# Optimization experiments

Hardware: AMD Instinct MI355X
Metric: run time of the kernel (lower is better)

## Reference

```python
import jax, jax.numpy as jnp
import numpy as np

# Static config (matches init_kwargs / spatial layout)
SHAPES = ((64, 64), (32, 32), (16, 16))   # (H, W) per level, bev=256 at /4,/8,/16
B, HEADS, LEVELS, POINTS, C = 2, 8, 3, 4, 256
HD = C // HEADS
NV = sum(h * w for h, w in SHAPES)        # 5376
NQ = NV
TP = HEADS * LEVELS * POINTS              # 96


def setup_inputs() -> dict:
    key = jax.random.key(0)
    ks = jax.random.split(key, 10)
    s = 1.0 / np.sqrt(C)
    inp = {
        'query': jax.random.normal(ks[0], (B, NQ, C), dtype=jnp.float32),
        'reference_points': jax.random.uniform(ks[1], (B, NQ, 2), dtype=jnp.float32),
        'value': jax.random.normal(ks[2], (B, NV, C), dtype=jnp.float32),
        'Wv': jax.random.normal(ks[3], (C, C), dtype=jnp.float32) * s,
        'bv': jnp.zeros((C,), dtype=jnp.float32),
        # offset proj: small scale so sampling stays local-ish (orig init is 0)
        'Woff': jax.random.normal(ks[4], (TP * 2, C), dtype=jnp.float32) * (0.02 * s),
        'boff': jnp.zeros((TP * 2,), dtype=jnp.float32),
        'Wa': jax.random.normal(ks[5], (TP, C), dtype=jnp.float32) * s,
        'ba': jnp.zeros((TP,), dtype=jnp.float32),
        'Wo': jax.random.normal(ks[6], (C, C), dtype=jnp.float32) * s,
        'bo': jnp.zeros((C,), dtype=jnp.float32),
    }
    return inp


def _msda(query, reference_points, value, Wv, bv, Woff, boff, Wa, ba, Wo, bo):
    Bb, nq, _ = query.shape
    # value projection -> per-head values
    v = (value @ Wv.T + bv).reshape(Bb, NV, HEADS, HD)
    # sampling offsets: (B, NQ, HEADS, LEVELS, POINTS, 2)
    off = (query @ Woff.T + boff).reshape(Bb, nq, HEADS, LEVELS, POINTS, 2)
    # attention weights: softmax over LEVELS*POINTS jointly
    a = (query @ Wa.T + ba).reshape(Bb, nq, HEADS, LEVELS * POINTS)
    a = jax.nn.softmax(a, axis=-1).reshape(Bb, nq, HEADS, LEVELS, POINTS)
    # sampling locations in [0,1] (clamp matches torch .clamp(0,1))
    loc = jnp.clip(reference_points[:, :, None, None, None, :] + off, 0.0, 1.0)

    out = jnp.zeros((Bb, HEADS, nq, HD), dtype=query.dtype)
    start = 0
    for lvl, (H, W) in enumerate(SHAPES):
        n = H * W
        # (B, HEADS, H*W, HD) flattened level feature map per head
        vl = jnp.transpose(v[:, start:start + n].reshape(Bb, H, W, HEADS, HD),
                           (0, 3, 1, 2, 4)).reshape(Bb, HEADS, n, HD)
        loc_l = loc[:, :, :, lvl]                     # (B, NQ, HEADS, K, 2)
        # align_corners=False unnormalization: ((g+1)*size - 1)/2 with g=2*loc-1
        x = loc_l[..., 0] * W - 0.5
        y = loc_l[..., 1] * H - 0.5
        x0 = jnp.floor(x)
        y0 = jnp.floor(y)
        wx1 = x - x0
        wy1 = y - y0
        x0i = x0.astype(jnp.int32)
        y0i = y0.astype(jnp.int32)
        acc = jnp.zeros((Bb, HEADS, nq * POINTS, HD), dtype=query.dtype)
        for dy in (0, 1):
            for dx in (0, 1):
                ix = x0i + dx
                iy = y0i + dy
                wgt = (wx1 if dx else 1.0 - wx1) * (wy1 if dy else 1.0 - wy1)
                # zero padding outside the map (padding_mode='zeros')
                valid = (ix >= 0) & (ix < W) & (iy >= 0) & (iy < H)
                idx = jnp.clip(iy, 0, H - 1) * W + jnp.clip(ix, 0, W - 1)
                idx_t = jnp.transpose(idx, (0, 2, 1, 3)).reshape(Bb, HEADS, nq * POINTS)
                g = jnp.take_along_axis(vl, idx_t[..., None], axis=2)  # (B,H,NQ*K,HD)
                w_t = jnp.transpose(wgt * valid.astype(wgt.dtype),
                                    (0, 2, 1, 3)).reshape(Bb, HEADS, nq * POINTS, 1)
                acc = acc + g * w_t
        aw = jnp.transpose(a[:, :, :, lvl], (0, 2, 1, 3)).reshape(Bb, HEADS, nq * POINTS, 1)
        out = out + (acc * aw).reshape(Bb, HEADS, nq, POINTS, HD).sum(axis=3)
        start += n
    out = jnp.transpose(out, (0, 2, 1, 3)).reshape(Bb, nq, C)
    return out @ Wo.T + bo


def reference(query, reference_points, value, Wv, bv, Woff, boff, Wa, ba, Wo, bo):
    return _msda(query, reference_points, value, Wv, bv, Woff, boff, Wa, ba, Wo, bo)
```

## Files before the change

### kernel.cpp

```cpp
#include <hip/hip_runtime.h>
#include <hip/hip_bf16.h>
#include <cmath>

#define BATCH   2
#define NQ      5376
#define NV      5376
#define CDIM    256
#define HEADS   8
#define HD      32
#define LEVELS  3
#define POINTS  4
#define TP      96
#define MROWS   (BATCH*NQ)
#define NOFF    (TP*2)
#define NQA     (NOFF+TP)

typedef __attribute__((ext_vector_type(8))) short bf16x8;
typedef __attribute__((ext_vector_type(4))) float f32x4;
typedef unsigned short u16;
typedef unsigned int   u32;

#define AS1 __attribute__((address_space(1)))
#define AS3 __attribute__((address_space(3)))

__device__ __forceinline__ void g2lds16(const void* g, void* l) {
    __builtin_amdgcn_global_load_lds((const AS1 void*)g, (AS3 void*)l, 16, 0, 0);
}

__device__ __forceinline__ u16 bf_of(float f) {
    union { __hip_bfloat16 h; u16 s; } u;
    u.h = __float2bfloat16(f);
    return u.s;
}
__device__ __forceinline__ float bf_back(u16 s) {
    return __uint_as_float((u32)s << 16);
}

__global__ __launch_bounds__(256) void split_vq_kernel(
    const float* __restrict__ value, const float* __restrict__ query,
    u16* __restrict__ vhi, u16* __restrict__ vlo,
    u16* __restrict__ qhi, int n4)
{
    int i = blockIdx.x * 256 + threadIdx.x;
    const float* src; u16* dh; u16* dl;
    if (i < n4) { src = value; dh = vhi; dl = vlo; }
    else        { src = query; dh = qhi; dl = nullptr; i -= n4; }
    const float4 v = reinterpret_cast<const float4*>(src)[i];
    ushort4 h;
    h.x = bf_of(v.x); h.y = bf_of(v.y); h.z = bf_of(v.z); h.w = bf_of(v.w);
    reinterpret_cast<ushort4*>(dh)[i] = h;
    if (dl) {
        ushort4 l;
        l.x = bf_of(v.x - bf_back(h.x));
        l.y = bf_of(v.y - bf_back(h.y));
        l.z = bf_of(v.z - bf_back(h.z));
        l.w = bf_of(v.w - bf_back(h.w));
        reinterpret_cast<ushort4*>(dl)[i] = l;
    }
}

__global__ __launch_bounds__(256) void split_w_kernel(
    const float* __restrict__ Wv, const float* __restrict__ Woff,
    const float* __restrict__ Wa, const float* __restrict__ Wo,
    u16* __restrict__ wv_hi, u16* __restrict__ wv_lo,
    u16* __restrict__ wqa_hi,
    u16* __restrict__ wo_hi, u16* __restrict__ wo_lo)
{
    const int i = blockIdx.x * 256 + threadIdx.x;
    const float* src; u16* dh; u16* dl; int j;
    if (i < 16384) {
        j = i; src = Wv + (size_t)j * 4; dh = wv_hi; dl = wv_lo;
    } else if (i < 34816) {
        j = i - 16384;
        const int row = j >> 6, c4 = j & 63;
        src = (row < NOFF) ? (Woff + (size_t)row * CDIM + c4 * 4)
                           : (Wa + (size_t)(row - NOFF) * CDIM + c4 * 4);
        dh = wqa_hi; dl = nullptr;
    } else {
        j = i - 34816; src = Wo + (size_t)j * 4; dh = wo_hi; dl = wo_lo;
    }
    const float4 v = *reinterpret_cast<const float4*>(src);
    ushort4 h;
    h.x = bf_of(v.x); h.y = bf_of(v.y); h.z = bf_of(v.z); h.w = bf_of(v.w);
    reinterpret_cast<ushort4*>(dh)[j] = h;
    if (dl) {
        ushort4 l;
        l.x = bf_of(v.x - bf_back(h.x));
        l.y = bf_of(v.y - bf_back(h.y));
        l.z = bf_of(v.z - bf_back(h.z));
        l.w = bf_of(v.w - bf_back(h.w));
        reinterpret_cast<ushort4*>(dl)[j] = l;
    }
}

#define GBM 64
#define GBN 64
#define GBK 32

template <int NPROD, int MODE>
__global__ __launch_bounds__(256) void gemm_split_kernel(
    const u16* __restrict__ Ah, const u16* __restrict__ Al,
    const u16* __restrict__ Bh, const u16* __restrict__ Bl,
    const float* __restrict__ bias, const float* __restrict__ bias2,
    void* __restrict__ Cout, void* __restrict__ Cout2,
    int M, int N, int K)
{
    __shared__ u16 sAh[GBM * GBK];
    __shared__ u16 sAl[GBM * GBK];
    __shared__ u16 sBh[GBN * GBK];
    __shared__ u16 sBl[GBN * GBK];

    const int m0 = blockIdx.x * GBM;
    const int n0 = blockIdx.y * GBN;
    const int tid  = threadIdx.x;
    const int lane = tid & 63;
    const int wave = tid >> 6;
    const int wr   = wave & 1;
    const int wc   = wave >> 1;
    const int qm   = lane & 15;
    const int quad = lane >> 4;

    f32x4 acc[2][2];
    #pragma unroll
    for (int i = 0; i < 2; ++i)
        #pragma unroll
        for (int j = 0; j < 2; ++j)
            acc[i][j] = (f32x4){0.f, 0.f, 0.f, 0.f};

    const int srow = (wave << 4) + (lane >> 2);
    const int sk   = (lane & 3) * 8;
    const int brc  = min(n0 + srow, N - 1);

    for (int k0 = 0; k0 < K; k0 += GBK) {
        const size_t ga = (size_t)(m0 + srow) * K + k0 + sk;
        const size_t gb = (size_t)brc * K + k0 + sk;
        g2lds16(Ah + ga, sAh + wave * 512);
        if (NPROD >= 2) g2lds16(Al + ga, sAl + wave * 512);
        g2lds16(Bh + gb, sBh + wave * 512);
        if (NPROD >= 3) g2lds16(Bl + gb, sBl + wave * 512);
        __syncthreads();

        bf16x8 fah[2], fal[2], fbh[2], fbl[2];
        #pragma unroll
        for (int x = 0; x < 2; ++x) {
            const int rm = wr * 32 + x * 16 + qm;
            const int rn = wc * 32 + x * 16 + qm;
            fah[x] = *reinterpret_cast<const bf16x8*>(&sAh[rm * GBK + quad * 8]);
            fbh[x] = *reinterpret_cast<const bf16x8*>(&sBh[rn * GBK + quad * 8]);
            if (NPROD >= 2)
                fal[x] = *reinterpret_cast<const bf16x8*>(&sAl[rm * GBK + quad * 8]);
            if (NPROD >= 3)
                fbl[x] = *reinterpret_cast<const bf16x8*>(&sBl[rn * GBK + quad * 8]);
        }
        #pragma unroll
        for (int mi = 0; mi < 2; ++mi)
            #pragma unroll
            for (int ni = 0; ni < 2; ++ni) {
                acc[mi][ni] = __builtin_amdgcn_mfma_f32_16x16x32_bf16(
                    fah[mi], fbh[ni], acc[mi][ni], 0, 0, 0);
                if (NPROD >= 2)
                    acc[mi][ni] = __builtin_amdgcn_mfma_f32_16x16x32_bf16(
                        fal[mi], fbh[ni], acc[mi][ni], 0, 0, 0);
                if (NPROD >= 3)
                    acc[mi][ni] = __builtin_amdgcn_mfma_f32_16x16x32_bf16(
                        fah[mi], fbl[ni], acc[mi][ni], 0, 0, 0);
            }
        __syncthreads();
    }

    #pragma unroll
    for (int mi = 0; mi < 2; ++mi) {
        #pragma unroll
        for (int ni = 0; ni < 2; ++ni) {
            const int n = n0 + wc * 32 + ni * 16 + qm;
            if (n >= N) continue;
            float bn;
            if (MODE == 2) bn = (n < NOFF) ? bias[n] : bias2[n - NOFF];
            else           bn = bias[n];
            #pragma unroll
            for (int r = 0; r < 4; ++r) {
                const int m = m0 + wr * 32 + mi * 16 + quad * 4 + r;
                const float val = acc[mi][ni][r] + bn;
                if (MODE == 0) {
                    reinterpret_cast<float*>(Cout)[(size_t)m * N + n] = val;
                } else if (MODE == 1) {
                    const int b = m / NV, rr = m - b * NV;
                    const int h = n >> 5, c = n & 31;
                    reinterpret_cast<u16*>(Cout)[
                        (((size_t)b * HEADS + h) * NV + rr) * HD + c] = bf_of(val);
                } else {
                    if (n < NOFF)
                        reinterpret_cast<float*>(Cout)[(size_t)m * NOFF + n] = val;
                    else
                        reinterpret_cast<float*>(Cout2)[(size_t)m * TP + (n - NOFF)] = val;
                }
            }
        }
    }
}

__global__ __launch_bounds__(256) void msda_core_kernel(
    const float* __restrict__ off,
    const float* __restrict__ alog,
    const float* __restrict__ refp,
    const u16*   __restrict__ v,
    u16* __restrict__ t_hi,
    u16* __restrict__ t_lo)
{
    const int tid  = threadIdx.x;
    const int half = tid >> 7;
    const int ht   = tid & 127;
    const int bq   = blockIdx.x * 2 + half;
    const int b    = bq / NQ;

    __shared__ float s_w[2][TP];
    __shared__ int   s_idx[2][TP][4];
    __shared__ float s_twt[2][TP][4];

    if (ht < TP) s_w[half][ht] = alog[(size_t)bq * TP + ht];
    __syncthreads();

    if (ht < HEADS) {
        float mx = -1e30f;
        #pragma unroll
        for (int i = 0; i < 12; ++i) mx = fmaxf(mx, s_w[half][ht * 12 + i]);
        float e[12];
        float sum = 0.f;
        #pragma unroll
        for (int i = 0; i < 12; ++i) {
            e[i] = expf(s_w[half][ht * 12 + i] - mx);
            sum += e[i];
        }
        const float inv = 1.f / sum;
        #pragma unroll
        for (int i = 0; i < 12; ++i) s_w[half][ht * 12 + i] = e[i] * inv;
    }
    __syncthreads();

    if (ht < TP) {
        const int j  = ht;
        const int jj = j % 12;
        const int l  = jj >> 2;
        const int Wl    = (l == 0) ? 64 : (l == 1) ? 32 : 16;
        const int start = (l == 0) ? 0 : (l == 1) ? 4096 : 5120;

        const float refx = refp[(size_t)bq * 2 + 0];
        const float refy = refp[(size_t)bq * 2 + 1];
        const float lx = fminf(fmaxf(refx + off[(size_t)bq * NOFF + j * 2 + 0], 0.f), 1.f) * (float)Wl - 0.5f;
        const float ly = fminf(fmaxf(refy + off[(size_t)bq * NOFF + j * 2 + 1], 0.f), 1.f) * (float)Wl - 0.5f;
        const float fx0 = floorf(lx), fy0 = floorf(ly);
        const int   x0  = (int)fx0,   y0  = (int)fy0;
        const float wx1 = lx - fx0,   wy1 = ly - fy0;
        const float wx0 = 1.f - wx1,  wy0 = 1.f - wy1;
        const float aw  = s_w[half][j];

        #pragma unroll
        for (int k = 0; k < 4; ++k) {
            const int dx = k & 1, dy = k >> 1;
            const int xi = x0 + dx, yi = y0 + dy;
            const bool ok = (xi >= 0) & (xi < Wl) & (yi >= 0) & (yi < Wl);
            const int xc = min(max(xi, 0), Wl - 1);
            const int yc = min(max(yi, 0), Wl - 1);
            s_idx[half][j][k] = (start + yc * Wl + xc) * (HD * 2);
            const float wxy = (dx ? wx1 : wx0) * (dy ? wy1 : wy0);
            s_twt[half][j][k] = ok ? aw * wxy : 0.f;
        }
    }
    __syncthreads();

    const int h   = ht >> 4;
    const int sub = ht & 15;
    const int q   = sub & 7;
    const int rep = sub >> 3;
    const char* vb = (const char*)v + (((size_t)b * HEADS + h) * NV) * (HD * 2) + q * 8;

    float acc0 = 0.f, acc1 = 0.f, acc2 = 0.f, acc3 = 0.f;
    #pragma unroll
    for (int g = 0; g < 3; ++g) {
        uint2 raw[8];
        float wt[8];
        #pragma unroll
        for (int pp = 0; pp < 2; ++pp) {
            const int j = h * 12 + rep * 6 + g * 2 + pp;
            const int4   ix = *reinterpret_cast<const int4*>(&s_idx[half][j][0]);
            const float4 tw = *reinterpret_cast<const float4*>(&s_twt[half][j][0]);
            raw[pp * 4 + 0] = *reinterpret_cast<const uint2*>(vb + ix.x);
            raw[pp * 4 + 1] = *reinterpret_cast<const uint2*>(vb + ix.y);
            raw[pp * 4 + 2] = *reinterpret_cast<const uint2*>(vb + ix.z);
            raw[pp * 4 + 3] = *reinterpret_cast<const uint2*>(vb + ix.w);
            wt[pp * 4 + 0] = tw.x; wt[pp * 4 + 1] = tw.y;
            wt[pp * 4 + 2] = tw.z; wt[pp * 4 + 3] = tw.w;
        }
        #pragma unroll
        for (int k = 0; k < 8; ++k) {
            acc0 += wt[k] * __uint_as_float(raw[k].x << 16);
            acc1 += wt[k] * __uint_as_float(raw[k].x & 0xffff0000u);
            acc2 += wt[k] * __uint_as_float(raw[k].y << 16);
            acc3 += wt[k] * __uint_as_float(raw[k].y & 0xffff0000u);
        }
    }

    acc0 += __shfl_xor(acc0, 8);
    acc1 += __shfl_xor(acc1, 8);
    acc2 += __shfl_xor(acc2, 8);
    acc3 += __shfl_xor(acc3, 8);

    if (rep == 0) {
        ushort4 hh, ll;
        hh.x = bf_of(acc0); ll.x = bf_of(acc0 - bf_back(hh.x));
        hh.y = bf_of(acc1); ll.y = bf_of(acc1 - bf_back(hh.y));
        hh.z = bf_of(acc2); ll.z = bf_of(acc2 - bf_back(hh.z));
        hh.w = bf_of(acc3); ll.w = bf_of(acc3 - bf_back(hh.w));
        const size_t base = (size_t)bq * CDIM + h * HD + q * 4;
        *reinterpret_cast<ushort4*>(t_hi + base) = hh;
        *reinterpret_cast<ushort4*>(t_lo + base) = ll;
    }
}

extern "C" void kernel_launch(void* const* d_in, const int* in_sizes, int n_in,
                              void* d_out, int out_size, void* d_ws, size_t ws_size,
                              hipStream_t stream)
{
    const float* query = (const float*)d_in[0];
    const float* refp  = (const float*)d_in[1];
    const float* value = (const float*)d_in[2];
    const float* Wv    = (const float*)d_in[3];
    const float* bv    = (const float*)d_in[4];
    const float* Woff  = (const float*)d_in[5];
    const float* boff  = (const float*)d_in[6];
    const float* Wa    = (const float*)d_in[7];
    const float* ba    = (const float*)d_in[8];
    const float* Wo    = (const float*)d_in[9];
    const float* bo    = (const float*)d_in[10];
    float* out = (float*)d_out;

    char* w = (char*)d_ws;
    const size_t SZ_QV = (size_t)MROWS * CDIM * 2;
    u16* q_hi   = (u16*)(w);
    u16* val_hi = (u16*)(w + 1 * SZ_QV);
    u16* val_lo = (u16*)(w + 2 * SZ_QV);
    u16* v_bf16 = (u16*)(w + 3 * SZ_QV);
    char* wp    = w + 4 * SZ_QV;
    u16* wv_hi  = (u16*)(wp);                  wp += (size_t)CDIM * CDIM * 2;
    u16* wv_lo  = (u16*)(wp);                  wp += (size_t)CDIM * CDIM * 2;
    u16* wqa_hi = (u16*)(wp);                  wp += (size_t)NQA * CDIM * 2;
    u16* wo_hi  = (u16*)(wp);                  wp += (size_t)CDIM * CDIM * 2;
    u16* wo_lo  = (u16*)(wp);                  wp += (size_t)CDIM * CDIM * 2;
    float* ws_off = (float*)(wp);              wp += (size_t)MROWS * NOFF * 4;
    float* ws_a   = (float*)(wp);
    u16* t_hi = val_hi;
    u16* t_lo = val_lo;

    const dim3 blk(256);
    const int n4_qv = MROWS * CDIM / 4;

    split_vq_kernel<<<dim3(2 * n4_qv / 256), blk, 0, stream>>>(
        value, query, val_hi, val_lo, q_hi, n4_qv);
    split_w_kernel<<<dim3(200), blk, 0, stream>>>(
        Wv, Woff, Wa, Wo, wv_hi, wv_lo, wqa_hi, wo_hi, wo_lo);

    gemm_split_kernel<2, 1><<<dim3(MROWS / GBM, CDIM / GBN), blk, 0, stream>>>(
        val_hi, val_lo, wv_hi, wv_lo, bv, nullptr, v_bf16, nullptr,
        MROWS, CDIM, CDIM);
    gemm_split_kernel<1, 2><<<dim3(MROWS / GBM, (NQA + GBN - 1) / GBN), blk, 0, stream>>>(
        q_hi, nullptr, wqa_hi, nullptr, boff, ba, ws_off, ws_a,
        MROWS, NQA, CDIM);
    msda_core_kernel<<<dim3(MROWS / 2), blk, 0, stream>>>(
        ws_off, ws_a, refp, v_bf16, t_hi, t_lo);
    gemm_split_kernel<2, 0><<<dim3(MROWS / GBM, CDIM / GBN), blk, 0, stream>>>(
        t_hi, t_lo, wo_hi, wo_lo, bo, nullptr, out, nullptr,
        MROWS, CDIM, CDIM);
}
```

Measured before the change: 141.9 us.

## Merge split kernels and fuse value and query projection GEMMs into one launch

Combines the two bf16 split kernels into a single launch, and runs the value projection GEMM and the offset/attention projection GEMM in one grid, choosing the job by block index. Each GEMM block is now indexed n-fastest, so blocks that share an A tile run close together. The value and output GEMMs no longer use the weight low-part product (NPROD 3 paths are gone; they were unused anyway since NPROD was 2). The aim is to remove launch overhead and the tail gaps between small kernels, at the cost of branch divergence at block level and a mixed workload within one grid.

Measured after the change: 140.6 us. About the same (-0.9%).

```diff
diff --git a/kernel.cpp b/kernel.cpp
--- a/kernel.cpp
+++ b/kernel.cpp
@@ -14,6 +14,7 @@
 #define MROWS   (BATCH*NQ)
 #define NOFF    (TP*2)
 #define NQA     (NOFF+TP)
+#define N4_VQ   (MROWS*CDIM/4)
 
 typedef __attribute__((ext_vector_type(8))) short bf16x8;
 typedef __attribute__((ext_vector_type(4))) float f32x4;
@@ -36,48 +37,31 @@
     return __uint_as_float((u32)s << 16);
 }
 
-__global__ __launch_bounds__(256) void split_vq_kernel(
+__global__ __launch_bounds__(256) void split_all_kernel(
     const float* __restrict__ value, const float* __restrict__ query,
-    u16* __restrict__ vhi, u16* __restrict__ vlo,
-    u16* __restrict__ qhi, int n4)
-{
-    int i = blockIdx.x * 256 + threadIdx.x;
-    const float* src; u16* dh; u16* dl;
-    if (i < n4) { src = value; dh = vhi; dl = vlo; }
-    else        { src = query; dh = qhi; dl = nullptr; i -= n4; }
-    const float4 v = reinterpret_cast<const float4*>(src)[i];
-    ushort4 h;
-    h.x = bf_of(v.x); h.y = bf_of(v.y); h.z = bf_of(v.z); h.w = bf_of(v.w);
-    reinterpret_cast<ushort4*>(dh)[i] = h;
-    if (dl) {
-        ushort4 l;
-        l.x = bf_of(v.x - bf_back(h.x));
-        l.y = bf_of(v.y - bf_back(h.y));
-        l.z = bf_of(v.z - bf_back(h.z));
-        l.w = bf_of(v.w - bf_back(h.w));
-        reinterpret_cast<ushort4*>(dl)[i] = l;
-    }
-}
-
-__global__ __launch_bounds__(256) void split_w_kernel(
     const float* __restrict__ Wv, const float* __restrict__ Woff,
     const float* __restrict__ Wa, const float* __restrict__ Wo,
+    u16* __restrict__ vhi, u16* __restrict__ vlo, u16* __restrict__ qhi,
     u16* __restrict__ wv_hi, u16* __restrict__ wv_lo,
     u16* __restrict__ wqa_hi,
     u16* __restrict__ wo_hi, u16* __restrict__ wo_lo)
 {
     const int i = blockIdx.x * 256 + threadIdx.x;
-    const float* src; u16* dh; u16* dl; int j;
-    if (i < 16384) {
-        j = i; src = Wv + (size_t)j * 4; dh = wv_hi; dl = wv_lo;
-    } else if (i < 34816) {
-        j = i - 16384;
+    int j; const float* src; u16 *dh, *dl;
+    if (i < N4_VQ) {
+        j = i; src = value + (size_t)j * 4; dh = vhi; dl = vlo;
+    } else if (i < 2 * N4_VQ) {
+        j = i - N4_VQ; src = query + (size_t)j * 4; dh = qhi; dl = nullptr;
+    } else if (i < 2 * N4_VQ + 16384) {
+        j = i - 2 * N4_VQ; src = Wv + (size_t)j * 4; dh = wv_hi; dl = wv_lo;
+    } else if (i < 2 * N4_VQ + 34816) {
+        j = i - 2 * N4_VQ - 16384;
         const int row = j >> 6, c4 = j & 63;
         src = (row < NOFF) ? (Woff + (size_t)row * CDIM + c4 * 4)
                            : (Wa + (size_t)(row - NOFF) * CDIM + c4 * 4);
         dh = wqa_hi; dl = nullptr;
     } else {
-        j = i - 34816; src = Wo + (size_t)j * 4; dh = wo_hi; dl = wo_lo;
+        j = i - 2 * N4_VQ - 34816; src = Wo + (size_t)j * 4; dh = wo_hi; dl = wo_lo;
     }
     const float4 v = *reinterpret_cast<const float4*>(src);
     ushort4 h;
@@ -98,20 +82,15 @@
 #define GBK 32
 
 template <int NPROD, int MODE>
-__global__ __launch_bounds__(256) void gemm_split_kernel(
+__device__ __forceinline__ void gemm_body(
+    int m0, int n0,
     const u16* __restrict__ Ah, const u16* __restrict__ Al,
     const u16* __restrict__ Bh, const u16* __restrict__ Bl,
     const float* __restrict__ bias, const float* __restrict__ bias2,
     void* __restrict__ Cout, void* __restrict__ Cout2,
-    int M, int N, int K)
-{
-    __shared__ u16 sAh[GBM * GBK];
-    __shared__ u16 sAl[GBM * GBK];
-    __shared__ u16 sBh[GBN * GBK];
-    __shared__ u16 sBl[GBN * GBK];
-
-    const int m0 = blockIdx.x * GBM;
-    const int n0 = blockIdx.y * GBN;
+    int N, int K,
+    u16* sAh, u16* sAl, u16* sBh, u16* sBl)
+{
     const int tid  = threadIdx.x;
     const int lane = tid & 63;
     const int wave = tid >> 6;
@@ -137,10 +116,9 @@
         g2lds16(Ah + ga, sAh + wave * 512);
         if (NPROD >= 2) g2lds16(Al + ga, sAl + wave * 512);
         g2lds16(Bh + gb, sBh + wave * 512);
-        if (NPROD >= 3) g2lds16(Bl + gb, sBl + wave * 512);
         __syncthreads();
 
-        bf16x8 fah[2], fal[2], fbh[2], fbl[2];
+        bf16x8 fah[2], fal[2], fbh[2];
         #pragma unroll
         for (int x = 0; x < 2; ++x) {
             const int rm = wr * 32 + x * 16 + qm;
@@ -149,8 +127,6 @@
             fbh[x] = *reinterpret_cast<const bf16x8*>(&sBh[rn * GBK + quad * 8]);
             if (NPROD >= 2)
                 fal[x] = *reinterpret_cast<const bf16x8*>(&sAl[rm * GBK + quad * 8]);
-            if (NPROD >= 3)
-                fbl[x] = *reinterpret_cast<const bf16x8*>(&sBl[rn * GBK + quad * 8]);
         }
         #pragma unroll
         for (int mi = 0; mi < 2; ++mi)
@@ -161,9 +137,6 @@
                 if (NPROD >= 2)
                     acc[mi][ni] = __builtin_amdgcn_mfma_f32_16x16x32_bf16(
                         fal[mi], fbh[ni], acc[mi][ni], 0, 0, 0);
-                if (NPROD >= 3)
-                    acc[mi][ni] = __builtin_amdgcn_mfma_f32_16x16x32_bf16(
-                        fah[mi], fbl[ni], acc[mi][ni], 0, 0, 0);
             }
         __syncthreads();
     }
@@ -199,6 +172,48 @@
     }
 }
 
+#define VBLOCKS (168 * 4)
+__global__ __launch_bounds__(256) void gemm_vqa_kernel(
+    const u16* __restrict__ vAh, const u16* __restrict__ vAl,
+    const u16* __restrict__ vBh, const float* __restrict__ vbias,
+    u16* __restrict__ vOut,
+    const u16* __restrict__ qAh, const u16* __restrict__ qBh,
+    const float* __restrict__ qb1, const float* __restrict__ qb2,
+    float* __restrict__ qOut1, float* __restrict__ qOut2)
+{
+    __shared__ u16 sAh[GBM * GBK];
+    __shared__ u16 sAl[GBM * GBK];
+    __shared__ u16 sBh[GBN * GBK];
+    const int bid = blockIdx.x;
+    if (bid < VBLOCKS) {
+        const int nt = bid & 3, mt = bid >> 2;
+        gemm_body<2, 1>(mt * GBM, nt * GBN, vAh, vAl, vBh, nullptr,
+                        vbias, nullptr, vOut, nullptr, CDIM, CDIM,
+                        sAh, sAl, sBh, nullptr);
+    } else {
+        const int b2 = bid - VBLOCKS;
+        const int nt = b2 % 5, mt = b2 / 5;
+        gemm_body<1, 2>(mt * GBM, nt * GBN, qAh, nullptr, qBh, nullptr,
+                        qb1, qb2, qOut1, qOut2, NQA, CDIM,
+                        sAh, sAl, sBh, nullptr);
+    }
+}
+
+__global__ __launch_bounds__(256) void gemm_out_kernel(
+    const u16* __restrict__ Ah, const u16* __restrict__ Al,
+    const u16* __restrict__ Bh, const float* __restrict__ bias,
+    float* __restrict__ Cout)
+{
+    __shared__ u16 sAh[GBM * GBK];
+    __shared__ u16 sAl[GBM * GBK];
+    __shared__ u16 sBh[GBN * GBK];
+    const int bid = blockIdx.x;
+    const int nt = bid & 3, mt = bid >> 2;
+    gemm_body<2, 0>(mt * GBM, nt * GBN, Ah, Al, Bh, nullptr,
+                    bias, nullptr, Cout, nullptr, CDIM, CDIM,
+                    sAh, sAl, sBh, nullptr);
+}
+
 __global__ __launch_bounds__(256) void msda_core_kernel(
     const float* __restrict__ off,
     const float* __restrict__ alog,
@@ -352,22 +367,18 @@
     u16* t_lo = val_lo;
 
     const dim3 blk(256);
-    const int n4_qv = MROWS * CDIM / 4;
-
-    split_vq_kernel<<<dim3(2 * n4_qv / 256), blk, 0, stream>>>(
-        value, query, val_hi, val_lo, q_hi, n4_qv);
-    split_w_kernel<<<dim3(200), blk, 0, stream>>>(
-        Wv, Woff, Wa, Wo, wv_hi, wv_lo, wqa_hi, wo_hi, wo_lo);
-
-    gemm_split_kernel<2, 1><<<dim3(MROWS / GBM, CDIM / GBN), blk, 0, stream>>>(
-        val_hi, val_lo, wv_hi, wv_lo, bv, nullptr, v_bf16, nullptr,
-        MROWS, CDIM, CDIM);
-    gemm_split_kernel<1, 2><<<dim3(MROWS / GBM, (NQA + GBN - 1) / GBN), blk, 0, stream>>>(
-        q_hi, nullptr, wqa_hi, nullptr, boff, ba, ws_off, ws_a,
-        MROWS, NQA, CDIM);
+
+    split_all_kernel<<<dim3((2 * N4_VQ + 51200) / 256), blk, 0, stream>>>(
+        value, query, Wv, Woff, Wa, Wo,
+        val_hi, val_lo, q_hi, wv_hi, wv_lo, wqa_hi, wo_hi, wo_lo);
+
+    gemm_vqa_kernel<<<dim3(VBLOCKS + (MROWS / GBM) * 5), blk, 0, stream>>>(
+        val_hi, val_lo, wv_hi, bv, v_bf16,
+        q_hi, wqa_hi, boff, ba, ws_off, ws_a);
+
     msda_core_kernel<<<dim3(MROWS / 2), blk, 0, stream>>>(
         ws_off, ws_a, refp, v_bf16, t_hi, t_lo);
-    gemm_split_kernel<2, 0><<<dim3(MROWS / GBM, CDIM / GBN), blk, 0, stream>>>(
-        t_hi, t_lo, wo_hi, wo_lo, bo, nullptr, out, nullptr,
-        MROWS, CDIM, CDIM);
-}
+
+    gemm_out_kernel<<<dim3((MROWS / GBM) * 4), blk, 0, stream>>>(
+        t_hi, t_lo, wo_hi, bo, out);
+}
```
